# Kernel tuning notes

Measured on AMD Instinct MI355X. Metric: run time of the kernel, lower is better.

Reference implementation:

```python
import jax, jax.numpy as jnp
import numpy as np

B, L, D, H, T = 64, 512, 768, 384, 9  # batch, seq_len, hidden, hidden//2, num_tags


def setup_inputs() -> dict:
    key = jax.random.key(0)
    ks = jax.random.split(key, 8)
    return {
        "encoder_out": jax.random.normal(ks[0], (B, L, D), jnp.float32),
        "ner_labels": jax.random.randint(ks[1], (B, L), 0, T),
        "mask": jnp.ones((B, L), jnp.bool_),
        "W1": jax.random.normal(ks[2], (D, H), jnp.float32) / np.sqrt(D).astype(np.float32),
        "b1": jnp.zeros((H,), jnp.float32),
        "W2": jax.random.normal(ks[3], (H, T), jnp.float32) / np.sqrt(H).astype(np.float32),
        "b2": jnp.zeros((T,), jnp.float32),
        "start_trans": jax.random.uniform(ks[4], (T,), jnp.float32, -0.1, 0.1),
        "end_trans": jax.random.uniform(ks[5], (T,), jnp.float32, -0.1, 0.1),
        "trans": jax.random.uniform(ks[6], (T, T), jnp.float32, -0.1, 0.1),
    }


def _crf_nll(emissions, tags, mask, start_trans, end_trans, trans):
    """-mean log-likelihood, matching pytorch-crf forward (reduction='mean')."""
    maskf = mask.astype(emissions.dtype)
    # ---- numerator: score of the gold tag path ----
    emit = jnp.take_along_axis(emissions, tags[..., None], axis=-1)[..., 0]  # [B,L]
    emit_score = jnp.sum(emit * maskf, axis=1)
    tr = trans[tags[:, :-1], tags[:, 1:]]  # [B,L-1]
    tr_score = jnp.sum(tr * maskf[:, 1:], axis=1)
    last_idx = jnp.sum(mask.astype(jnp.int32), axis=1) - 1
    last_tags = jnp.take_along_axis(tags, last_idx[:, None], axis=1)[:, 0]
    numer = start_trans[tags[:, 0]] + emit_score + tr_score + end_trans[last_tags]
    # ---- denominator: forward algorithm (log partition) via scan ----
    alpha0 = start_trans[None, :] + emissions[:, 0]          # [B,T]
    em_rest = jnp.swapaxes(emissions[:, 1:], 0, 1)           # [L-1,B,T]
    mk_rest = jnp.swapaxes(maskf[:, 1:], 0, 1)               # [L-1,B]

    def step(alpha, xs):
        e_t, m_t = xs
        nxt = jax.nn.logsumexp(alpha[:, :, None] + trans[None, :, :] + e_t[:, None, :], axis=1)
        return jnp.where(m_t[:, None] > 0, nxt, alpha), None

    alpha, _ = jax.lax.scan(step, alpha0, (em_rest, mk_rest))
    denom = jax.nn.logsumexp(alpha + end_trans[None, :], axis=1)
    return -jnp.mean(numer - denom)


def reference(encoder_out, ner_labels, mask, W1, b1, W2, b2, start_trans, end_trans, trans):
    # proj: Linear -> GELU (exact erf, torch default) -> Dropout (identity in eval)
    h = jax.nn.gelu(encoder_out @ W1 + b1, approximate=False)
    emissions = h @ W2 + b2  # [B,L,T]
    return _crf_nll(emissions, ner_labels, mask, start_trans, end_trans, trans)
```

## Files before the change

kernel.cpp:

```cpp
#include <hip/hip_runtime.h>
#include <hip/hip_bf16.h>
#include <math.h>

#define B_ 64
#define L_ 512
#define D_ 768
#define H_ 384
#define T_ 9
#define M_ (B_ * L_)

typedef __attribute__((ext_vector_type(8))) short short8;
typedef __attribute__((ext_vector_type(4))) float f32x4;

__device__ __forceinline__ unsigned short f2bf(float f) {
    unsigned u = __float_as_uint(f);
    u += 0x7FFFu + ((u >> 16) & 1u);
    return (unsigned short)(u >> 16);
}

__device__ __forceinline__ unsigned pkbf2(float a, float b) {
    __hip_bfloat162 h = __float22bfloat162_rn(float2{a, b});
    return *(unsigned*)&h;
}

__device__ __forceinline__ float gelu_fast(float x) {
    float z2 = 1.5957691216f * x + 0.0713548162726f * x * x * x;
    return x / (1.f + __expf(-z2));
}

__device__ __forceinline__ float wredf(float v) {
#pragma unroll
    for (int m = 32; m >= 1; m >>= 1) v += __shfl_xor(v, m, 64);
    return v;
}

__global__ __launch_bounds__(256) void prep_kernel(
    const float* __restrict__ W1, const float* __restrict__ W2,
    unsigned short* __restrict__ W1F, unsigned short* __restrict__ W2F,
    float* __restrict__ out)
{
    if (blockIdx.x == 0 && threadIdx.x == 0) out[0] = 0.f;
    const int g    = blockIdx.x * 4 + (threadIdx.x >> 6);
    const int lane = threadIdx.x & 63;
    const int lm   = lane & 15;
    const int q    = lane >> 4;
    if (g < 576) {
        const int nt = g / 24;
        const int kc = g - nt * 24;
        const int n  = nt * 16 + lm;
        short8 v;
#pragma unroll
        for (int j = 0; j < 8; ++j)
            v[j] = (short)f2bf(W1[(size_t)(kc * 32 + q * 8 + j) * H_ + n]);
        *(short8*)(W1F + ((size_t)g * 64 + lane) * 8) = v;
    } else if (g < 588) {
        const int kk = g - 576;
        short8 v;
#pragma unroll
        for (int j = 0; j < 8; ++j) {
            int k = kk * 32 + q * 8 + j;
            v[j] = (lm < 9) ? (short)f2bf(W2[(size_t)k * T_ + lm]) : (short)0;
        }
        *(short8*)(W2F + ((size_t)kk * 64 + lane) * 8) = v;
    }
}

__global__ __launch_bounds__(256, 2) void emis_mfma_kernel(
    const float* __restrict__ X,
    const unsigned short* __restrict__ W1F,
    const float* __restrict__ b1,
    const unsigned short* __restrict__ W2F,
    const float* __restrict__ b2,
    float* __restrict__ em)
{
    __shared__ unsigned short Hs[64 * 392];

    const int t    = threadIdx.x;
    const int lane = t & 63;
    const int w    = t >> 6;
    const int lm   = lane & 15;
    const int q    = lane >> 4;
    const int row0 = blockIdx.x * 64;

    const float* xa[4];
#pragma unroll
    for (int mt = 0; mt < 4; ++mt)
        xa[mt] = X + (size_t)(row0 + mt * 16 + lm) * D_ + (q << 3);

    const unsigned short* bp[6];
#pragma unroll
    for (int i = 0; i < 6; ++i)
        bp[i] = W1F + ((size_t)(w * 6 + i) * 24 * 64 + lane) * 8;

    f32x4 acc[4][6];
#pragma unroll
    for (int mt = 0; mt < 4; ++mt)
#pragma unroll
        for (int i = 0; i < 6; ++i) acc[mt][i] = (f32x4)0.f;

#pragma unroll
    for (int kc = 0; kc < 24; ++kc) {
        short8 af[4];
#pragma unroll
        for (int mt = 0; mt < 4; ++mt) {
            float4 a0 = *(const float4*)(xa[mt] + kc * 32);
            float4 a1 = *(const float4*)(xa[mt] + kc * 32 + 4);
            int4 iv = {(int)pkbf2(a0.x, a0.y), (int)pkbf2(a0.z, a0.w),
                       (int)pkbf2(a1.x, a1.y), (int)pkbf2(a1.z, a1.w)};
            af[mt] = *(short8*)&iv;
        }
        short8 bf[6];
#pragma unroll
        for (int i = 0; i < 6; ++i)
            bf[i] = *(const short8*)(bp[i] + (size_t)kc * 512);
#pragma unroll
        for (int mt = 0; mt < 4; ++mt)
#pragma unroll
            for (int i = 0; i < 6; ++i)
                acc[mt][i] = __builtin_amdgcn_mfma_f32_16x16x32_bf16(
                    af[mt], bf[i], acc[mt][i], 0, 0, 0);
    }

#pragma unroll
    for (int i = 0; i < 6; ++i) {
        const int col = w * 96 + i * 16 + lm;
        const float b1v = b1[col];
#pragma unroll
        for (int mt = 0; mt < 4; ++mt)
#pragma unroll
            for (int r = 0; r < 4; ++r) {
                float h = gelu_fast(acc[mt][i][r] + b1v);
                Hs[(mt * 16 + q * 4 + r) * 392 + col] = f2bf(h);
            }
    }
    __syncthreads();

    f32x4 e = (f32x4)0.f;
#pragma unroll
    for (int kk = 0; kk < 12; ++kk) {
        short8 ah = *(const short8*)&Hs[(w * 16 + lm) * 392 + kk * 32 + (q << 3)];
        short8 bw = *(const short8*)(W2F + ((size_t)(kk * 64 + lane)) * 8);
        e = __builtin_amdgcn_mfma_f32_16x16x32_bf16(ah, bw, e, 0, 0, 0);
    }
    if (lm < 9) {
        const float b2v = b2[lm];
#pragma unroll
        for (int r = 0; r < 4; ++r)
            em[(size_t)(row0 + w * 16 + q * 4 + r) * T_ + lm] = e[r] + b2v;
    }
}

__global__ __launch_bounds__(576) void crf_kernel(
    const float* __restrict__ em,
    const int* __restrict__ labels,
    const unsigned char* __restrict__ maskb,
    const float* __restrict__ st,
    const float* __restrict__ et,
    const float* __restrict__ tr,
    float* __restrict__ out)
{
    const int b = blockIdx.x;
    const int t = threadIdx.x;

    __shared__ float es[64 * 73];
    __shared__ float Ms[64 * 81];
    __shared__ float trs[81];
    __shared__ float red[2];
    __shared__ unsigned char msh[L_];
    __shared__ int lbs[L_];

    const int mstride =
        (maskb[0] != 0 && maskb[1] == 0 && maskb[2] == 0 && maskb[3] == 0) ? 4 : 1;

    const float* eb = em + (size_t)b * L_ * T_;
    for (int i = t; i < L_ * T_; i += 576) {
        int tt = i / T_, j = i - tt * T_;
        es[(tt >> 3) * 73 + (tt & 7) * 9 + j] = eb[i];
    }
    if (t < 81) trs[t] = tr[t];
    for (int i = t; i < L_; i += 576) {
        msh[i] = maskb[((size_t)b * L_ + i) * (size_t)mstride];
        lbs[i] = labels[b * L_ + i];
    }
    __syncthreads();

    {
        const int c  = t / 9;
        const int i0 = t - c * 9;
        float trr[81];
#pragma unroll
        for (int i = 0; i < 81; ++i) trr[i] = trs[i];
        float V[9];
#pragma unroll
        for (int j = 0; j < 9; ++j) V[j] = (j == i0) ? 0.f : -1e30f;

        const int sbeg = (c == 0) ? 1 : 0;
        for (int s = sbeg; s < 8; ++s) {
            int tt = c * 8 + s;
            if (msh[tt]) {
                const float* ep = &es[c * 73 + s * 9];
                float nv[9];
#pragma unroll
                for (int j = 0; j < 9; ++j) {
                    float a[9];
#pragma unroll
                    for (int k = 0; k < 9; ++k) a[k] = V[k] + trr[k * 9 + j];
                    float mx = a[0];
#pragma unroll
                    for (int k = 1; k < 9; ++k) mx = fmaxf(mx, a[k]);
                    float sum = 0.f;
#pragma unroll
                    for (int k = 0; k < 9; ++k) sum += __expf(a[k] - mx);
                    nv[j] = ep[j] + mx + __logf(sum);
                }
#pragma unroll
                for (int j = 0; j < 9; ++j) V[j] = nv[j];
            }
        }
#pragma unroll
        for (int j = 0; j < 9; ++j) Ms[c * 81 + i0 * 9 + j] = V[j];
    }
    __syncthreads();

    const int lane = t & 63;
    const int w    = t >> 6;
    if (w == 0) {
        const int jj = lane < 9 ? lane : 8;
        float alpha = (lane < 9) ? st[jj] + es[jj] : -1e30f;
        for (int c = 0; c < 64; ++c) {
            float a[9];
#pragma unroll
            for (int i = 0; i < 9; ++i) {
                float av = __shfl(alpha, i, 64);
                a[i] = av + Ms[c * 81 + i * 9 + jj];
            }
            float mx = a[0];
#pragma unroll
            for (int i = 1; i < 9; ++i) mx = fmaxf(mx, a[i]);
            float sum = 0.f;
#pragma unroll
            for (int i = 0; i < 9; ++i) sum += __expf(a[i] - mx);
            float nv = mx + __logf(sum);
            if (lane < 9) alpha = nv;
        }
        float v = (lane < 9) ? alpha + et[jj] : -1e30f;
        float mx = v;
#pragma unroll
        for (int m = 32; m >= 1; m >>= 1) mx = fmaxf(mx, __shfl_xor(mx, m, 64));
        float s = __expf(v - mx);
        s = wredf(s);
        if (lane == 0) red[0] = mx + __logf(s);
    } else if (w == 1) {
        float emit_s = 0.f, tr_sc = 0.f, mcnt = 0.f;
        for (int tt = lane; tt < L_; tt += 64) {
            if (msh[tt]) {
                mcnt += 1.f;
                int tag = lbs[tt];
                emit_s += es[(tt >> 3) * 73 + (tt & 7) * 9 + tag];
                if (tt >= 1) tr_sc += trs[lbs[tt - 1] * 9 + tag];
            }
        }
        emit_s = wredf(emit_s);
        tr_sc  = wredf(tr_sc);
        mcnt   = wredf(mcnt);
        if (lane == 0) {
            int last = (int)mcnt - 1;
            red[1] = st[lbs[0]] + emit_s + tr_sc + et[lbs[last]];
        }
    }
    __syncthreads();
    if (t == 0) atomicAdd(out, (red[0] - red[1]) * (1.0f / (float)B_));
}

extern "C" void kernel_launch(void* const* d_in, const int* in_sizes, int n_in,
                              void* d_out, int out_size, void* d_ws, size_t ws_size,
                              hipStream_t stream) {
    const float*         enc    = (const float*)d_in[0];
    const int*           labels = (const int*)d_in[1];
    const unsigned char* mask   = (const unsigned char*)d_in[2];
    const float*         W1     = (const float*)d_in[3];
    const float*         b1     = (const float*)d_in[4];
    const float*         W2     = (const float*)d_in[5];
    const float*         b2     = (const float*)d_in[6];
    const float*         st     = (const float*)d_in[7];
    const float*         et     = (const float*)d_in[8];
    const float*         tr     = (const float*)d_in[9];

    float* em           = (float*)d_ws;
    unsigned short* W1F = (unsigned short*)(em + (size_t)M_ * T_);
    unsigned short* W2F = W1F + (size_t)576 * 64 * 8;

    prep_kernel<<<147, 256, 0, stream>>>(W1, W2, W1F, W2F, (float*)d_out);
    emis_mfma_kernel<<<M_ / 64, 256, 0, stream>>>(enc, W1F, b1, W2F, b2, em);
    crf_kernel<<<B_, 576, 0, stream>>>(em, labels, mask, st, et, tr, (float*)d_out);
}
```

Before: 262.1 us.

## Stage X tiles through double-buffered LDS with register prefetch in emission GEMM

Each X element is now loaded once per block and converted to bf16 by one thread into a shared LDS A tile, so the four waves no longer each reload and convert the same rows from global memory. The K loop is split into 8 stages of 96 columns, with LDS double-buffering and register prefetch two stages ahead to overlap global loads with MFMA work. This costs a barrier per stage, more live registers for the prefetched float4s, and extra LDS traffic, all under the existing 2-blocks-per-SM launch bound.

```diff
diff --git a/kernel.cpp b/kernel.cpp
--- a/kernel.cpp
+++ b/kernel.cpp
@@ -32,6 +32,10 @@
 #pragma unroll
     for (int m = 32; m >= 1; m >>= 1) v += __shfl_xor(v, m, 64);
     return v;
+}
+
+__device__ __forceinline__ void sync_lds() {
+    asm volatile("s_waitcnt lgkmcnt(0)\n\ts_barrier" ::: "memory");
 }
 
 __global__ __launch_bounds__(256) void prep_kernel(
@@ -73,7 +77,8 @@
     const float* __restrict__ b2,
     float* __restrict__ em)
 {
-    __shared__ unsigned short Hs[64 * 392];
+    __shared__ unsigned short Sh[64 * 392];
+    unsigned short* As = Sh;
 
     const int t    = threadIdx.x;
     const int lane = t & 63;
@@ -82,44 +87,71 @@
     const int q    = lane >> 4;
     const int row0 = blockIdx.x * 64;
 
-    const float* xa[4];
+    const int ar  = t >> 2;
+    const int ako = (t & 3) << 3;
+    const float* xp = X + (size_t)(row0 + ar) * D_ + ako;
+
+    f32x4 acc[4][6];
 #pragma unroll
     for (int mt = 0; mt < 4; ++mt)
-        xa[mt] = X + (size_t)(row0 + mt * 16 + lm) * D_ + (q << 3);
-
-    const unsigned short* bp[6];
-#pragma unroll
-    for (int i = 0; i < 6; ++i)
-        bp[i] = W1F + ((size_t)(w * 6 + i) * 24 * 64 + lane) * 8;
-
-    f32x4 acc[4][6];
-#pragma unroll
-    for (int mt = 0; mt < 4; ++mt)
 #pragma unroll
         for (int i = 0; i < 6; ++i) acc[mt][i] = (f32x4)0.f;
 
 #pragma unroll
-    for (int kc = 0; kc < 24; ++kc) {
-        short8 af[4];
-#pragma unroll
-        for (int mt = 0; mt < 4; ++mt) {
-            float4 a0 = *(const float4*)(xa[mt] + kc * 32);
-            float4 a1 = *(const float4*)(xa[mt] + kc * 32 + 4);
-            int4 iv = {(int)pkbf2(a0.x, a0.y), (int)pkbf2(a0.z, a0.w),
-                       (int)pkbf2(a1.x, a1.y), (int)pkbf2(a1.z, a1.w)};
-            af[mt] = *(short8*)&iv;
-        }
-        short8 bf[6];
-#pragma unroll
-        for (int i = 0; i < 6; ++i)
-            bf[i] = *(const short8*)(bp[i] + (size_t)kc * 512);
-#pragma unroll
-        for (int mt = 0; mt < 4; ++mt)
-#pragma unroll
-            for (int i = 0; i < 6; ++i)
-                acc[mt][i] = __builtin_amdgcn_mfma_f32_16x16x32_bf16(
-                    af[mt], bf[i], acc[mt][i], 0, 0, 0);
-    }
+    for (int c = 0; c < 3; ++c) {
+        float4 p0 = *(const float4*)(xp + c * 32);
+        float4 p1 = *(const float4*)(xp + c * 32 + 4);
+        int4 v = {(int)pkbf2(p0.x, p0.y), (int)pkbf2(p0.z, p0.w),
+                  (int)pkbf2(p1.x, p1.y), (int)pkbf2(p1.z, p1.w)};
+        *(int4*)&As[(size_t)(c * 64 + ar) * 40 + ako] = v;
+    }
+    float4 xv[2][3][2];
+#pragma unroll
+    for (int c = 0; c < 3; ++c) {
+        xv[0][c][0] = *(const float4*)(xp + (3 + c) * 32);
+        xv[0][c][1] = *(const float4*)(xp + (3 + c) * 32 + 4);
+        xv[1][c][0] = *(const float4*)(xp + (6 + c) * 32);
+        xv[1][c][1] = *(const float4*)(xp + (6 + c) * 32 + 4);
+    }
+
+#pragma unroll
+    for (int st = 0; st < 8; ++st) {
+        const int s = st & 1;
+        sync_lds();
+#pragma unroll
+        for (int c = 0; c < 3; ++c) {
+            short8 af[4];
+#pragma unroll
+            for (int mt = 0; mt < 4; ++mt)
+                af[mt] = *(const short8*)&As[(size_t)((s * 3 + c) * 64 + mt * 16 + lm) * 40 + (q << 3)];
+#pragma unroll
+            for (int i = 0; i < 6; ++i) {
+                short8 bf = *(const short8*)(W1F +
+                    (((size_t)(w * 6 + i) * 24 + st * 3 + c) * 64 + lane) * 8);
+#pragma unroll
+                for (int mt = 0; mt < 4; ++mt)
+                    acc[mt][i] = __builtin_amdgcn_mfma_f32_16x16x32_bf16(
+                        af[mt], bf, acc[mt][i], 0, 0, 0);
+            }
+        }
+        if (st < 7) {
+#pragma unroll
+            for (int c = 0; c < 3; ++c) {
+                float4 x0 = xv[s][c][0], x1 = xv[s][c][1];
+                int4 v = {(int)pkbf2(x0.x, x0.y), (int)pkbf2(x0.z, x0.w),
+                          (int)pkbf2(x1.x, x1.y), (int)pkbf2(x1.z, x1.w)};
+                *(int4*)&As[(size_t)(((s ^ 1) * 3 + c) * 64 + ar) * 40 + ako] = v;
+            }
+            if (st < 6) {
+#pragma unroll
+                for (int c = 0; c < 3; ++c) {
+                    xv[s][c][0] = *(const float4*)(xp + ((st + 2) * 3 + c) * 32);
+                    xv[s][c][1] = *(const float4*)(xp + ((st + 2) * 3 + c) * 32 + 4);
+                }
+            }
+        }
+    }
+    __syncthreads();
 
 #pragma unroll
     for (int i = 0; i < 6; ++i) {
@@ -130,7 +162,7 @@
 #pragma unroll
             for (int r = 0; r < 4; ++r) {
                 float h = gelu_fast(acc[mt][i][r] + b1v);
-                Hs[(mt * 16 + q * 4 + r) * 392 + col] = f2bf(h);
+                Sh[(mt * 16 + q * 4 + r) * 392 + col] = f2bf(h);
             }
     }
     __syncthreads();
@@ -138,7 +170,7 @@
     f32x4 e = (f32x4)0.f;
 #pragma unroll
     for (int kk = 0; kk < 12; ++kk) {
-        short8 ah = *(const short8*)&Hs[(w * 16 + lm) * 392 + kk * 32 + (q << 3)];
+        short8 ah = *(const short8*)&Sh[(w * 16 + lm) * 392 + kk * 32 + (q << 3)];
         short8 bw = *(const short8*)(W2F + ((size_t)(kk * 64 + lane)) * 8);
         e = __builtin_amdgcn_mfma_f32_16x16x32_bf16(ah, bw, e, 0, 0, 0);
     }
```

After: 233.2 us. 11.0% less time.
